# Performance work log

Measured on AMD Instinct MI355X. Metric: run time of the kernel, lower is better.

Reference implementation:

```python
import jax, jax.numpy as jnp
import numpy as np

POOLED = 7      # kernel_size
SCALE = 0.25    # spatial_scale
GMAX = 2        # upper bound of adaptive sampling grid (box sizes chosen so ceil(roi/7) <= 2)


def setup_inputs() -> dict:
    key = jax.random.key(0)
    k1, k2, k3, k4, k5, k6 = jax.random.split(key, 6)
    B, C, H, W, K = 4, 256, 128, 128, 1000
    features = jax.random.normal(k1, (B, C, H, W), dtype=jnp.float32)
    img = H / SCALE  # 512.0: image-space extent
    bidx = jax.random.randint(k2, (K,), 0, B).astype(jnp.float32)
    bw = jax.random.uniform(k3, (K,), minval=8.0, maxval=56.0)
    bh = jax.random.uniform(k4, (K,), minval=8.0, maxval=56.0)
    x1 = jax.random.uniform(k5, (K,), minval=0.0, maxval=img - 56.0)
    y1 = jax.random.uniform(k6, (K,), minval=0.0, maxval=img - 56.0)
    boxes = jnp.stack([bidx, x1, y1, x1 + bw, y1 + bh], axis=1)
    return {"features": features, "boxes": boxes}


def _sample_coords(start, bin_sz, grid):
    # start/bin_sz/grid: [K] -> coords [K, POOLED, GMAX]
    p = jnp.arange(POOLED, dtype=jnp.float32)
    i = jnp.arange(GMAX, dtype=jnp.float32)
    return (start[:, None, None] + p[None, :, None] * bin_sz[:, None, None]
            + (i[None, None, :] + 0.5) * bin_sz[:, None, None] / grid[:, None, None])


def roi_align(features, boxes):
    B, C, H, W = features.shape
    K = boxes.shape[0]
    b = boxes[:, 0].astype(jnp.int32)
    x1, y1, x2, y2 = (boxes[:, i] * SCALE for i in (1, 2, 3, 4))
    # aligned=False: no -0.5 offset, clamp roi size to >= 1
    roi_w = jnp.maximum(x2 - x1, 1.0)
    roi_h = jnp.maximum(y2 - y1, 1.0)
    bin_w = roi_w / POOLED
    bin_h = roi_h / POOLED
    # sampling_ratio = -1 -> adaptive grid = ceil(roi_size / pooled)
    gh = jnp.ceil(roi_h / POOLED)
    gw = jnp.ceil(roi_w / POOLED)

    y = _sample_coords(y1, bin_h, gh)  # [K,7,GMAX]
    x = _sample_coords(x1, bin_w, gw)  # [K,7,GMAX]
    vy = (jnp.arange(GMAX)[None, None, :] < gh[:, None, None])  # [K,1,GMAX]
    vx = (jnp.arange(GMAX)[None, None, :] < gw[:, None, None])

    # full sample grid [K, 7, GMAX, 7, GMAX] -> flatten to [K, P]
    shp = (K, POOLED, GMAX, POOLED, GMAX)
    Y = jnp.broadcast_to(y[:, :, :, None, None], shp).reshape(K, -1)
    X = jnp.broadcast_to(x[:, None, None, :, :], shp).reshape(K, -1)
    V = jnp.broadcast_to(vy[:, :, :, None, None] & vx[:, None, None, :, :], shp).reshape(K, -1)

    # bilinear interpolation, torchvision boundary semantics
    inval = (Y < -1.0) | (Y > H) | (X < -1.0) | (X > W)
    Yc = jnp.clip(Y, 0.0)
    Xc = jnp.clip(X, 0.0)
    yl = jnp.minimum(Yc.astype(jnp.int32), H - 1)
    xl = jnp.minimum(Xc.astype(jnp.int32), W - 1)
    yh = jnp.minimum(yl + 1, H - 1)
    xh = jnp.minimum(xl + 1, W - 1)
    Yc = jnp.where(yl >= H - 1, yl.astype(jnp.float32), Yc)
    Xc = jnp.where(xl >= W - 1, xl.astype(jnp.float32), Xc)
    ly = Yc - yl
    lx = Xc - xl
    hy = 1.0 - ly
    hx = 1.0 - lx
    m = jnp.where(inval | (~V), 0.0, 1.0)
    w1 = hy * hx * m; w2 = hy * lx * m; w3 = ly * hx * m; w4 = ly * lx * m

    def gather(yi, xi):
        # advanced indexing: [K,P] indices -> [K,P,C]
        return features[b[:, None], :, yi, xi]

    val = (w1[..., None] * gather(yl, xl) + w2[..., None] * gather(yl, xh)
           + w3[..., None] * gather(yh, xl) + w4[..., None] * gather(yh, xh))  # [K,P,C]
    val = val.reshape(K, POOLED, GMAX, POOLED, GMAX, C)
    out = val.sum(axis=(2, 4)) / (gh * gw)[:, None, None, None]  # [K,7,7,C]
    return jnp.transpose(out, (0, 3, 1, 2))  # [K,C,7,7]


def reference(features, boxes):
    return roi_align(features, boxes)
```

## Files before the change

kernel.cpp:

```cpp
#include <hip/hip_runtime.h>

#define POOLED 7
#define SCALE  0.25f
#define CCH    256
#define HH     128
#define WW     128
#define HW     (HH * WW)

#define NCH      16
#define NCHUNK   2
#define NBLK_PER_BOX (CCH / (NCH * NCHUNK))
#define PATCH_H  15
#define PATCH_W  16
#define PIXROW   17
#define NPIX     (14 * PIXROW + 16)
#define CHPAD    20

__global__ __launch_bounds__(256) void roi_align_kernel(
    const float* __restrict__ feat,
    const float* __restrict__ boxes,
    float* __restrict__ out,
    int K)
{
    __shared__ float patch[NPIX * CHPAD];

    int bx = blockIdx.x;
    int k  = bx >> 3;
    int cb = (bx & 7) * (NCH * NCHUNK);
    if (k >= K) return;
    int t = threadIdx.x;

    const float* box = boxes + (size_t)k * 5;
    int   b  = (int)box[0];
    float x1 = box[1] * SCALE;
    float y1 = box[2] * SCALE;
    float x2 = box[3] * SCALE;
    float y2 = box[4] * SCALE;

    float roi_w = fmaxf(x2 - x1, 1.0f);
    float roi_h = fmaxf(y2 - y1, 1.0f);
    float bin_w = roi_w * (1.0f / POOLED);
    float bin_h = roi_h * (1.0f / POOLED);
    int gw = (int)ceilf(roi_w * (1.0f / POOLED));
    int gh = (int)ceilf(roi_h * (1.0f / POOLED));
    float inv_gh = 1.0f / (float)gh;
    float inv_gw = 1.0f / (float)gw;
    int ns = gh * gw;

    float ymin = y1 + 0.5f * bin_h * inv_gh;
    float ymax = y1 + 6 * bin_h + ((gh - 1) + 0.5f) * bin_h * inv_gh;
    float xmin = x1 + 0.5f * bin_w * inv_gw;

    int ylo = min((int)fmaxf(ymin, 0.0f), HH - 1);
    int xlo = min((int)fmaxf(xmin, 0.0f), WW - 1);
    int ylmax = min((int)fmaxf(ymax, 0.0f), HH - 1);
    int h_p = min(ylmax + 1, HH - 1) - ylo + 1;
    if (h_p > PATCH_H) h_p = PATCH_H;

    int p  = t & 63;
    int pc = min(p, 48);
    int pw = pc % POOLED;
    int ph = pc / POOLED;
    int c4 = t >> 6;

    float wa[4], wb[4], wc_[4], wd[4];
    int   oa[4], ob[4], oc[4], od[4];

#pragma unroll
    for (int s = 0; s < 4; ++s) {
        if (s >= ns) break;
        int iy = s % gh;
        int ix = s / gh;

        float y = y1 + ph * bin_h + (iy + 0.5f) * bin_h * inv_gh;
        float x = x1 + pw * bin_w + (ix + 0.5f) * bin_w * inv_gw;
        bool valid = (y >= -1.0f) && (y <= (float)HH) && (x >= -1.0f) && (x <= (float)WW);

        float yc = fmaxf(y, 0.0f);
        int yl = min((int)yc, HH - 1);
        int yh2 = min(yl + 1, HH - 1);
        float ly = (yl >= HH - 1) ? 0.0f : (yc - (float)yl);
        float hy = 1.0f - ly;

        float xc = fmaxf(x, 0.0f);
        int xl = min((int)xc, WW - 1);
        int xh2 = min(xl + 1, WW - 1);
        float lx = (xl >= WW - 1) ? 0.0f : (xc - (float)xl);
        float hx = 1.0f - lx;

        float m = valid ? 1.0f : 0.0f;
        wa[s]  = hy * hx * m;
        wb[s]  = hy * lx * m;
        wc_[s] = ly * hx * m;
        wd[s]  = ly * lx * m;

        int ry  = max(0, min(yl  - ylo, h_p - 1));
        int ryh = max(0, min(yh2 - ylo, h_p - 1));
        int rxl = max(0, min(xl  - xlo, PATCH_W - 1));
        int rxh = max(0, min(xh2 - xlo, PATCH_W - 1));
        oa[s] = (ry  * PIXROW + rxl) * CHPAD;
        ob[s] = (ry  * PIXROW + rxh) * CHPAD;
        oc[s] = (ryh * PIXROW + rxl) * CHPAD;
        od[s] = (ryh * PIXROW + rxh) * CHPAD;
    }

    int lch  = t >> 4;
    int lcol = t & 15;
    int xcol = min(xlo + lcol, WW - 1);
    float sc = inv_gh * inv_gw;

    for (int ch = 0; ch < NCHUNK; ++ch) {
        if (ch) __syncthreads();

        {
            const float* g = feat + ((size_t)b * CCH + cb + ch * NCH + lch) * HW + xcol;
            float* lp = patch + lcol * CHPAD + lch;
            for (int r = 0; r < h_p; ++r) {
                lp[r * (PIXROW * CHPAD)] = g[(ylo + r) * WW];
            }
        }
        __syncthreads();

        if (p < 49) {
            float4 acc = {0.0f, 0.0f, 0.0f, 0.0f};
            const float* cp = patch + c4 * 4;
#pragma unroll
            for (int s = 0; s < 4; ++s) {
                if (s >= ns) break;
                float4 va = *(const float4*)(cp + oa[s]);
                float4 vb = *(const float4*)(cp + ob[s]);
                float4 vc = *(const float4*)(cp + oc[s]);
                float4 vd = *(const float4*)(cp + od[s]);
                float w1 = wa[s], w2 = wb[s], w3 = wc_[s], w4 = wd[s];
                acc.x += w1 * va.x + w2 * vb.x + w3 * vc.x + w4 * vd.x;
                acc.y += w1 * va.y + w2 * vb.y + w3 * vc.y + w4 * vd.y;
                acc.z += w1 * va.z + w2 * vb.z + w3 * vc.z + w4 * vd.z;
                acc.w += w1 * va.w + w2 * vb.w + w3 * vc.w + w4 * vd.w;
            }
            float* obase = out + ((size_t)k * CCH + cb + ch * NCH + c4 * 4) * 49 + p;
            obase[0]      = acc.x * sc;
            obase[49]     = acc.y * sc;
            obase[2 * 49] = acc.z * sc;
            obase[3 * 49] = acc.w * sc;
        }
    }
}

extern "C" void kernel_launch(void* const* d_in, const int* in_sizes, int n_in,
                              void* d_out, int out_size, void* d_ws, size_t ws_size,
                              hipStream_t stream) {
    const float* feat  = (const float*)d_in[0];
    const float* boxes = (const float*)d_in[1];
    float* out = (float*)d_out;

    int K = in_sizes[1] / 5;
    int blocks = K * NBLK_PER_BOX;
    roi_align_kernel<<<blocks, 256, 0, stream>>>(feat, boxes, out, K);
}
```

Before: 133.0 us.

## Pair boxes per block, sort boxes by image/quadrant, vectorize and prefetch patch loads

Adds a single-block pre-pass that buckets boxes by batch index and image quadrant so neighbouring blocks touch nearby feature regions and share cache. Each block now handles two boxes. The global patch loads become float4 reads aligned to a 4-column boundary, and the next chunk's load is issued before the current chunk is computed so memory latency overlaps the bilinear work. Sample weights are built from separable y/x terms assuming at most a 2x2 grid. The trade-offs are an extra kernel launch, heavy macro code, and more registers held live per thread.

After: 132.4 us. Within noise of the previous version (-0.4%).

```diff
diff --git a/kernel.cpp b/kernel.cpp
--- a/kernel.cpp
+++ b/kernel.cpp
@@ -8,142 +8,264 @@
 #define HW     (HH * WW)
 
 #define NCH      16
-#define NCHUNK   2
-#define NBLK_PER_BOX (CCH / (NCH * NCHUNK))
 #define PATCH_H  15
-#define PATCH_W  16
-#define PIXROW   17
-#define NPIX     (14 * PIXROW + 16)
+#define NV       5
+#define PIXROW   19
+#define NPIX     (PATCH_H * PIXROW)
 #define CHPAD    20
+#define ROWSTR   (PIXROW * CHPAD)
+
+__global__ void box_sort_kernel(const float* __restrict__ boxes,
+                                int* __restrict__ perm, int K)
+{
+    __shared__ int hist[16];
+    __shared__ int base[16];
+    int t = threadIdx.x;
+    if (t < 16) hist[t] = 0;
+    __syncthreads();
+    for (int i = t; i < K; i += blockDim.x) {
+        const float* bp = boxes + i * 5;
+        int key = (((int)bp[0] & 3) << 2)
+                | ((bp[2] >= 256.0f) ? 2 : 0)
+                | ((bp[1] >= 256.0f) ? 1 : 0);
+        atomicAdd(&hist[key], 1);
+    }
+    __syncthreads();
+    if (t == 0) {
+        int acc = 0;
+        for (int j = 0; j < 16; ++j) { base[j] = acc; acc += hist[j]; }
+    }
+    __syncthreads();
+    for (int i = t; i < K; i += blockDim.x) {
+        const float* bp = boxes + i * 5;
+        int key = (((int)bp[0] & 3) << 2)
+                | ((bp[2] >= 256.0f) ? 2 : 0)
+                | ((bp[1] >= 256.0f) ? 1 : 0);
+        int pos = atomicAdd(&base[key], 1);
+        perm[pos] = i;
+    }
+}
 
 __global__ __launch_bounds__(256) void roi_align_kernel(
     const float* __restrict__ feat,
     const float* __restrict__ boxes,
     float* __restrict__ out,
+    const int* __restrict__ perm,
     int K)
 {
-    __shared__ float patch[NPIX * CHPAD];
+    __shared__ __align__(16) float patch[NPIX * CHPAD];
 
     int bx = blockIdx.x;
-    int k  = bx >> 3;
-    int cb = (bx & 7) * (NCH * NCHUNK);
-    if (k >= K) return;
+    int pq = bx >> 3;
+    int cb = (bx & 7) * (NCH * 2);
+    int kAi = 2 * pq;
+    if (kAi >= K) return;
+    int kBi = min(kAi + 1, K - 1);
+    int kA = perm ? perm[kAi] : kAi;
+    int kB = perm ? perm[kBi] : kBi;
     int t = threadIdx.x;
 
-    const float* box = boxes + (size_t)k * 5;
-    int   b  = (int)box[0];
-    float x1 = box[1] * SCALE;
-    float y1 = box[2] * SCALE;
-    float x2 = box[3] * SCALE;
-    float y2 = box[4] * SCALE;
-
-    float roi_w = fmaxf(x2 - x1, 1.0f);
-    float roi_h = fmaxf(y2 - y1, 1.0f);
-    float bin_w = roi_w * (1.0f / POOLED);
-    float bin_h = roi_h * (1.0f / POOLED);
-    int gw = (int)ceilf(roi_w * (1.0f / POOLED));
-    int gh = (int)ceilf(roi_h * (1.0f / POOLED));
-    float inv_gh = 1.0f / (float)gh;
-    float inv_gw = 1.0f / (float)gw;
-    int ns = gh * gw;
-
-    float ymin = y1 + 0.5f * bin_h * inv_gh;
-    float ymax = y1 + 6 * bin_h + ((gh - 1) + 0.5f) * bin_h * inv_gh;
-    float xmin = x1 + 0.5f * bin_w * inv_gw;
-
-    int ylo = min((int)fmaxf(ymin, 0.0f), HH - 1);
-    int xlo = min((int)fmaxf(xmin, 0.0f), WW - 1);
-    int ylmax = min((int)fmaxf(ymax, 0.0f), HH - 1);
-    int h_p = min(ylmax + 1, HH - 1) - ylo + 1;
-    if (h_p > PATCH_H) h_p = PATCH_H;
+    const float* bpA = boxes + kA * 5;
+    const float* bpB = boxes + kB * 5;
+    float bA0 = bpA[0], bA1 = bpA[1], bA2 = bpA[2], bA3 = bpA[3], bA4 = bpA[4];
+    float bB0 = bpB[0], bB1 = bpB[1], bB2 = bpB[2], bB3 = bpB[3], bB4 = bpB[4];
 
     int p  = t & 63;
     int pc = min(p, 48);
     int pw = pc % POOLED;
     int ph = pc / POOLED;
-    int c4 = t >> 6;
+    int cg = t >> 6;
+    int lch = t >> 4;
+    int sub = t & 15;
+
+#define CALC_GEOM(S, B0, B1, B2, B3, B4)                                      \
+    int s_b##S, s_ylo##S, s_x4##S, s_hp##S, s_mcr##S, s_ns##S, ghm##S;        \
+    float x1##S, y1##S, bin_w##S, bin_h##S, inv_gh##S, inv_gw##S, sc##S;      \
+    {                                                                         \
+        x1##S = (B1) * SCALE; y1##S = (B2) * SCALE;                           \
+        float x2 = (B3) * SCALE, y2 = (B4) * SCALE;                           \
+        float roi_w = fmaxf(x2 - x1##S, 1.0f);                                \
+        float roi_h = fmaxf(y2 - y1##S, 1.0f);                                \
+        bin_w##S = roi_w * (1.0f / POOLED);                                   \
+        bin_h##S = roi_h * (1.0f / POOLED);                                   \
+        int gw = (int)ceilf(roi_w * (1.0f / POOLED));                         \
+        int gh = (int)ceilf(roi_h * (1.0f / POOLED));                         \
+        inv_gh##S = 1.0f / (float)gh; inv_gw##S = 1.0f / (float)gw;           \
+        sc##S = inv_gh##S * inv_gw##S;                                        \
+        float ymin = y1##S + 0.5f * bin_h##S * inv_gh##S;                     \
+        float ymax = y1##S + 6 * bin_h##S                                     \
+                   + ((gh - 1) + 0.5f) * bin_h##S * inv_gh##S;                \
+        float xmin = x1##S + 0.5f * bin_w##S * inv_gw##S;                     \
+        int ylo = min((int)fmaxf(ymin, 0.0f), HH - 1);                        \
+        int xlo = min((int)fmaxf(xmin, 0.0f), WW - 1);                        \
+        int xlo4 = xlo & ~3;                                                  \
+        int ylmax = min((int)fmaxf(ymax, 0.0f), HH - 1);                      \
+        int h_p = min(ylmax + 1, HH - 1) - ylo + 1;                           \
+        if (h_p > PATCH_H) h_p = PATCH_H;                                     \
+        int mcr = min(WW - 1 - xlo4, (xlo - xlo4) + 14);                      \
+        s_b##S   = __builtin_amdgcn_readfirstlane((int)(B0));                 \
+        s_ylo##S = __builtin_amdgcn_readfirstlane(ylo);                       \
+        s_x4##S  = __builtin_amdgcn_readfirstlane(xlo4);                      \
+        s_hp##S  = __builtin_amdgcn_readfirstlane(h_p);                       \
+        s_mcr##S = __builtin_amdgcn_readfirstlane(mcr);                       \
+        s_ns##S  = __builtin_amdgcn_readfirstlane(gh * gw);                   \
+        ghm##S   = __builtin_amdgcn_readfirstlane(gh - 1);                    \
+    }
+
+#define CALC_SMAP(S)                                                          \
+    bool act##S[NV], actw##S[NV];                                             \
+    int  goff##S[NV], la##S[NV];                                              \
+    const float* gch##S = feat + (s_b##S * CCH + cb + lch) * HW;              \
+    {                                                                         \
+        int lim = s_hp##S * NV;                                               \
+        _Pragma("unroll")                                                     \
+        for (int i = 0; i < NV; ++i) {                                        \
+            int idx = i * 16 + sub;                                           \
+            int r = idx / NV;                                                 \
+            int v = idx - r * NV;                                             \
+            act##S[i]  = (idx < lim) && (4 * v <= s_mcr##S);                  \
+            actw##S[i] = act##S[i] && (v < 4);                                \
+            goff##S[i] = (s_ylo##S + r) * WW + min(s_x4##S + 4 * v, WW - 4);  \
+            la##S[i]   = (r * PIXROW + 4 * v) * CHPAD + lch;                  \
+        }                                                                     \
+    }
+
+#define YSIDE(S, IYC, HY, LY, RT, RHT) {                                      \
+        float y = yb + IYC * bin_h##S * inv_gh##S;                            \
+        bool vld = (y >= -1.0f) && (y <= (float)HH);                          \
+        float yc = fmaxf(y, 0.0f);                                            \
+        int yl = min((int)yc, HH - 1);                                        \
+        int yh2 = min(yl + 1, HH - 1);                                        \
+        float ly = (yl >= HH - 1) ? 0.0f : (yc - (float)yl);                  \
+        HY = vld ? (1.0f - ly) : 0.0f;                                        \
+        LY = vld ? ly : 0.0f;                                                 \
+        int ry  = max(0, min(yl  - s_ylo##S, s_hp##S - 1));                   \
+        int ryh = max(0, min(yh2 - s_ylo##S, s_hp##S - 1));                   \
+        RT  = ry  * ROWSTR;                                                   \
+        RHT = ryh * ROWSTR;                                                   \
+    }
+#define XSIDE(S, IXC, HX, LX, RT, RHT) {                                      \
+        float x = xb + IXC * bin_w##S * inv_gw##S;                            \
+        bool vld = (x >= -1.0f) && (x <= (float)WW);                          \
+        float xc = fmaxf(x, 0.0f);                                            \
+        int xl = min((int)xc, WW - 1);                                        \
+        int xh2 = min(xl + 1, WW - 1);                                        \
+        float lx = (xl >= WW - 1) ? 0.0f : (xc - (float)xl);                  \
+        HX = vld ? (1.0f - lx) : 0.0f;                                        \
+        LX = vld ? lx : 0.0f;                                                 \
+        int rxl = max(0, min(xl  - s_x4##S, PIXROW - 1));                     \
+        int rxh = max(0, min(xh2 - s_x4##S, PIXROW - 1));                     \
+        RT  = rxl * CHPAD;                                                    \
+        RHT = rxh * CHPAD;                                                    \
+    }
 
     float wa[4], wb[4], wc_[4], wd[4];
     int   oa[4], ob[4], oc[4], od[4];
 
-#pragma unroll
-    for (int s = 0; s < 4; ++s) {
-        if (s >= ns) break;
-        int iy = s % gh;
-        int ix = s / gh;
-
-        float y = y1 + ph * bin_h + (iy + 0.5f) * bin_h * inv_gh;
-        float x = x1 + pw * bin_w + (ix + 0.5f) * bin_w * inv_gw;
-        bool valid = (y >= -1.0f) && (y <= (float)HH) && (x >= -1.0f) && (x <= (float)WW);
-
-        float yc = fmaxf(y, 0.0f);
-        int yl = min((int)yc, HH - 1);
-        int yh2 = min(yl + 1, HH - 1);
-        float ly = (yl >= HH - 1) ? 0.0f : (yc - (float)yl);
-        float hy = 1.0f - ly;
-
-        float xc = fmaxf(x, 0.0f);
-        int xl = min((int)xc, WW - 1);
-        int xh2 = min(xl + 1, WW - 1);
-        float lx = (xl >= WW - 1) ? 0.0f : (xc - (float)xl);
-        float hx = 1.0f - lx;
-
-        float m = valid ? 1.0f : 0.0f;
-        wa[s]  = hy * hx * m;
-        wb[s]  = hy * lx * m;
-        wc_[s] = ly * hx * m;
-        wd[s]  = ly * lx * m;
-
-        int ry  = max(0, min(yl  - ylo, h_p - 1));
-        int ryh = max(0, min(yh2 - ylo, h_p - 1));
-        int rxl = max(0, min(xl  - xlo, PATCH_W - 1));
-        int rxh = max(0, min(xh2 - xlo, PATCH_W - 1));
-        oa[s] = (ry  * PIXROW + rxl) * CHPAD;
-        ob[s] = (ry  * PIXROW + rxh) * CHPAD;
-        oc[s] = (ryh * PIXROW + rxl) * CHPAD;
-        od[s] = (ryh * PIXROW + rxh) * CHPAD;
-    }
-
-    int lch  = t >> 4;
-    int lcol = t & 15;
-    int xcol = min(xlo + lcol, WW - 1);
-    float sc = inv_gh * inv_gw;
-
-    for (int ch = 0; ch < NCHUNK; ++ch) {
-        if (ch) __syncthreads();
-
-        {
-            const float* g = feat + ((size_t)b * CCH + cb + ch * NCH + lch) * HW + xcol;
-            float* lp = patch + lcol * CHPAD + lch;
-            for (int r = 0; r < h_p; ++r) {
-                lp[r * (PIXROW * CHPAD)] = g[(ylo + r) * WW];
-            }
-        }
-        __syncthreads();
-
-        if (p < 49) {
-            float4 acc = {0.0f, 0.0f, 0.0f, 0.0f};
-            const float* cp = patch + c4 * 4;
-#pragma unroll
-            for (int s = 0; s < 4; ++s) {
-                if (s >= ns) break;
-                float4 va = *(const float4*)(cp + oa[s]);
-                float4 vb = *(const float4*)(cp + ob[s]);
-                float4 vc = *(const float4*)(cp + oc[s]);
-                float4 vd = *(const float4*)(cp + od[s]);
-                float w1 = wa[s], w2 = wb[s], w3 = wc_[s], w4 = wd[s];
-                acc.x += w1 * va.x + w2 * vb.x + w3 * vc.x + w4 * vd.x;
-                acc.y += w1 * va.y + w2 * vb.y + w3 * vc.y + w4 * vd.y;
-                acc.z += w1 * va.z + w2 * vb.z + w3 * vc.z + w4 * vd.z;
-                acc.w += w1 * va.w + w2 * vb.w + w3 * vc.w + w4 * vd.w;
-            }
-            float* obase = out + ((size_t)k * CCH + cb + ch * NCH + c4 * 4) * 49 + p;
-            obase[0]      = acc.x * sc;
-            obase[49]     = acc.y * sc;
-            obase[2 * 49] = acc.z * sc;
-            obase[3 * 49] = acc.w * sc;
-        }
-    }
+#define CALC_WEIGHTS(S) {                                                     \
+    float yb = y1##S + ph * bin_h##S;                                         \
+    float xb = x1##S + pw * bin_w##S;                                         \
+    float hy0, ly0, hy1, ly1;                                                 \
+    int   ryT0, ryhT0, ryT1, ryhT1;                                           \
+    float hx0, lx0, hx1, lx1;                                                 \
+    int   rxT0, rxhT0, rxT1, rxhT1;                                           \
+    YSIDE(S, 0.5f, hy0, ly0, ryT0, ryhT0)                                     \
+    YSIDE(S, 1.5f, hy1, ly1, ryT1, ryhT1)                                     \
+    XSIDE(S, 0.5f, hx0, lx0, rxT0, rxhT0)                                     \
+    XSIDE(S, 1.5f, hx1, lx1, rxT1, rxhT1)                                     \
+    wa[0] = hy0*hx0; wb[0] = hy0*lx0; wc_[0] = ly0*hx0; wd[0] = ly0*lx0;      \
+    oa[0] = ryT0+rxT0;  ob[0] = ryT0+rxhT0;                                   \
+    oc[0] = ryhT0+rxT0; od[0] = ryhT0+rxhT0;                                  \
+    {                                                                         \
+        float hyS = ghm##S ? hy1 : hy0, lyS = ghm##S ? ly1 : ly0;             \
+        int ryS = ghm##S ? ryT1 : ryT0, ryhS = ghm##S ? ryhT1 : ryhT0;        \
+        float hxS = ghm##S ? hx0 : hx1, lxS = ghm##S ? lx0 : lx1;             \
+        int rxS = ghm##S ? rxT0 : rxT1, rxhS = ghm##S ? rxhT0 : rxhT1;        \
+        wa[1] = hyS*hxS; wb[1] = hyS*lxS; wc_[1] = lyS*hxS; wd[1] = lyS*lxS;  \
+        oa[1] = ryS+rxS;  ob[1] = ryS+rxhS;                                   \
+        oc[1] = ryhS+rxS; od[1] = ryhS+rxhS;                                  \
+    }                                                                         \
+    wa[2] = hy0*hx1; wb[2] = hy0*lx1; wc_[2] = ly0*hx1; wd[2] = ly0*lx1;      \
+    oa[2] = ryT0+rxT1;  ob[2] = ryT0+rxhT1;                                   \
+    oc[2] = ryhT0+rxT1; od[2] = ryhT0+rxhT1;                                  \
+    wa[3] = hy1*hx1; wb[3] = hy1*lx1; wc_[3] = ly1*hx1; wd[3] = ly1*lx1;      \
+    oa[3] = ryT1+rxT1;  ob[3] = ryT1+rxhT1;                                   \
+    oc[3] = ryhT1+rxT1; od[3] = ryhT1+rxhT1;                                  \
+}
+
+#define ISSUE(S, C) {                                                         \
+    const float* g = gch##S + (C) * (NCH * HW);                               \
+    _Pragma("unroll")                                                         \
+    for (int i = 0; i < NV; ++i)                                              \
+        if (act##S[i]) u[i] = *(const float4*)(g + goff##S[i]);               \
+}
+
+#define LDSW(S) {                                                             \
+    _Pragma("unroll")                                                         \
+    for (int i = 0; i < NV; ++i)                                              \
+        if (act##S[i]) {                                                      \
+            float* lp = patch + la##S[i];                                     \
+            lp[0]         = u[i].x;                                           \
+            lp[CHPAD]     = u[i].y;                                           \
+            lp[2 * CHPAD] = u[i].z;                                           \
+            if (actw##S[i]) lp[3 * CHPAD] = u[i].w;                           \
+        }                                                                     \
+}
+
+#define BILIN(SS) {                                                           \
+        float4 va = *(const float4*)(cp + oa[SS]);                            \
+        float4 vb = *(const float4*)(cp + ob[SS]);                            \
+        float4 vc = *(const float4*)(cp + oc[SS]);                            \
+        float4 vd = *(const float4*)(cp + od[SS]);                            \
+        float w1 = wa[SS], w2 = wb[SS], w3 = wc_[SS], w4 = wd[SS];            \
+        acc.x += w1 * va.x + w2 * vb.x + w3 * vc.x + w4 * vd.x;               \
+        acc.y += w1 * va.y + w2 * vb.y + w3 * vc.y + w4 * vd.y;               \
+        acc.z += w1 * va.z + w2 * vb.z + w3 * vc.z + w4 * vd.z;               \
+        acc.w += w1 * va.w + w2 * vb.w + w3 * vc.w + w4 * vd.w;               \
+    }
+#define COMPUTE(S, KIDX, CHB) {                                               \
+        float4 acc = {0.0f, 0.0f, 0.0f, 0.0f};                                \
+        const float* cp = patch + cg * 4;                                     \
+        BILIN(0)                                                              \
+        if (s_ns##S > 1) BILIN(1)                                             \
+        if (s_ns##S > 2) { BILIN(2) BILIN(3) }                                \
+        int ob_ = ((KIDX) * CCH + cb + (CHB) + cg * 4) * 49 + p;              \
+        out[ob_]          = acc.x * sc##S;                                    \
+        out[ob_ + 49]     = acc.y * sc##S;                                    \
+        out[ob_ + 2 * 49] = acc.z * sc##S;                                    \
+        out[ob_ + 3 * 49] = acc.w * sc##S;                                    \
+    }
+
+    CALC_GEOM(A, bA0, bA1, bA2, bA3, bA4)
+    CALC_SMAP(A)
+    float4 u[NV];
+    ISSUE(A, 0)
+    CALC_WEIGHTS(A)
+
+    LDSW(A)
+    ISSUE(A, 1)
+    __syncthreads();
+    if (p < 49) COMPUTE(A, kA, 0)
+
+    CALC_GEOM(B, bB0, bB1, bB2, bB3, bB4)
+    CALC_SMAP(B)
+    __syncthreads();
+    LDSW(A)
+    ISSUE(B, 0)
+    __syncthreads();
+    if (p < 49) COMPUTE(A, kA, NCH)
+
+    CALC_WEIGHTS(B)
+    __syncthreads();
+    LDSW(B)
+    ISSUE(B, 1)
+    __syncthreads();
+    if (p < 49) COMPUTE(B, kB, 0)
+
+    __syncthreads();
+    LDSW(B)
+    __syncthreads();
+    if (p < 49) COMPUTE(B, kB, NCH)
 }
 
 extern "C" void kernel_launch(void* const* d_in, const int* in_sizes, int n_in,
@@ -154,6 +276,12 @@
     float* out = (float*)d_out;
 
     int K = in_sizes[1] / 5;
-    int blocks = K * NBLK_PER_BOX;
-    roi_align_kernel<<<blocks, 256, 0, stream>>>(feat, boxes, out, K);
-}
+    int* perm = nullptr;
+    if (d_ws && ws_size >= (size_t)K * sizeof(int)) {
+        perm = (int*)d_ws;
+        box_sort_kernel<<<1, 1024, 0, stream>>>(boxes, perm, K);
+    }
+    int pairs = (K + 1) / 2;
+    int blocks = pairs * 8;
+    roi_align_kernel<<<blocks, 256, 0, stream>>>(feat, boxes, out, perm, K);
+}
```
